# Performance work log

Measured on AMD Instinct MI355X. Metric: run time of the kernel, lower is better.

## Reference

```python
import jax, jax.numpy as jnp
import numpy as np

B, S, DIN = 1, 2048, 4096
H, KV, DH = 32, 8, 128          # num_heads, num_kv_groups, head_dim
G = H // KV                      # group_size


def setup_inputs() -> dict:
    key = jax.random.key(0)
    ks = jax.random.split(key, 6)
    input_tensor = jax.random.normal(ks[0], (B, S, DIN), jnp.float32)
    # boolean mask: True = masked out. Causal upper-triangular mask.
    attention_mask = jnp.triu(jnp.ones((S, S), bool), k=1)[None, None]
    # RoPE tables (context_len, head_dim), rotate-half layout
    inv_freq = 1.0 / (10000.0 ** (jnp.arange(0, DH, 2, dtype=jnp.float32) / DH))
    ang = jnp.arange(S, dtype=jnp.float32)[:, None] * inv_freq[None, :]  # (S, DH/2)
    ang = jnp.concatenate([ang, ang], axis=-1)                            # (S, DH)
    cos, sin = jnp.cos(ang), jnp.sin(ang)
    scale = 0.02
    Wq = jax.random.normal(ks[1], (DIN, H * DH), jnp.float32) * scale
    Wk = jax.random.normal(ks[2], (DIN, KV * DH), jnp.float32) * scale
    Wv = jax.random.normal(ks[3], (DIN, KV * DH), jnp.float32) * scale
    Wo = jax.random.normal(ks[4], (H * DH, DIN), jnp.float32) * scale
    return {"input_tensor": input_tensor, "attention_mask": attention_mask,
            "cos": cos, "sin": sin, "Wq": Wq, "Wk": Wk, "Wv": Wv, "Wo": Wo}


def _rope(t, cos, sin):
    # t: (B, heads, S, DH); cos/sin: (S, DH)
    t1, t2 = jnp.split(t, 2, axis=-1)
    rot = jnp.concatenate([-t2, t1], axis=-1)
    return t * cos[None, None] + rot * sin[None, None]


def reference(input_tensor, attention_mask, cos, sin, Wq, Wk, Wv, Wo):
    b, s, _ = input_tensor.shape
    q = (input_tensor @ Wq).reshape(b, s, H, DH).transpose(0, 2, 1, 3)   # (B,H,S,DH)
    k = (input_tensor @ Wk).reshape(b, s, KV, DH).transpose(0, 2, 1, 3)  # (B,KV,S,DH)
    v = (input_tensor @ Wv).reshape(b, s, KV, DH).transpose(0, 2, 1, 3)
    q = _rope(q, cos, sin)
    k = _rope(k, cos, sin)
    # GQA: duplicate each kv head across its group of query heads
    k = jnp.repeat(k, G, axis=1)  # (B,H,S,DH)
    v = jnp.repeat(v, G, axis=1)
    scores = jnp.einsum('bhqd,bhkd->bhqk', q, k)
    scores = jnp.where(attention_mask, -jnp.inf, scores)
    weights = jax.nn.softmax(scores / np.float32(np.sqrt(DH)), axis=-1)
    ctx = jnp.einsum('bhqk,bhkd->bhqd', weights, v)
    ctx = ctx.transpose(0, 2, 1, 3).reshape(b, s, H * DH)
    return ctx @ Wo
```

## Files before the change

### kernel.cpp

```cpp
#include <hip/hip_runtime.h>
#include <hip/hip_bf16.h>
#include <stdint.h>
#include <stddef.h>

typedef __attribute__((ext_vector_type(8))) short bf16x8;
typedef __attribute__((ext_vector_type(8))) unsigned short u16x8;
typedef __attribute__((ext_vector_type(4))) float f32x4;
typedef __attribute__((ext_vector_type(16))) float f32x16;

#define MFMA16(a, b, c) __builtin_amdgcn_mfma_f32_16x16x32_bf16((a), (b), (c), 0, 0, 0)
#define MFMA32(a, b, c) __builtin_amdgcn_mfma_f32_32x32x16_bf16((a), (b), (c), 0, 0, 0)

__device__ __forceinline__ unsigned short f2b(float f) {
  union { float f; unsigned u; } v; v.f = f;
  unsigned r = v.u + 0x7fffu + ((v.u >> 16) & 1u);
  return (unsigned short)(r >> 16);
}
__device__ __forceinline__ float b2f(unsigned short h) {
  union { unsigned u; float f; } v; v.u = ((unsigned)h) << 16;
  return v.f;
}

__device__ __forceinline__ void gload_lds16(const void* g, void* l) {
  __builtin_amdgcn_global_load_lds((const __attribute__((address_space(1))) void*)g,
                                   (__attribute__((address_space(3))) void*)l, 16, 0, 0);
}

__global__ void k_transpose_f32_bf16(const float* __restrict__ in,
                                     unsigned short* __restrict__ out,
                                     int K, int N) {
  __shared__ float tile[64][65];
  const int kb = blockIdx.x * 64;
  const int nb = blockIdx.y * 64;
  const int t = threadIdx.x;
  const int c4 = (t & 15) * 4;
  const int rr = t >> 4;
#pragma unroll
  for (int i = 0; i < 4; ++i) {
    int r = rr + i * 16;
    float4 v = *reinterpret_cast<const float4*>(in + (size_t)(kb + r) * N + nb + c4);
    tile[r][c4 + 0] = v.x; tile[r][c4 + 1] = v.y;
    tile[r][c4 + 2] = v.z; tile[r][c4 + 3] = v.w;
  }
  __syncthreads();
#pragma unroll
  for (int i = 0; i < 4; ++i) {
    int n = rr + i * 16;
    ushort4 w;
    w.x = f2b(tile[c4 + 0][n]); w.y = f2b(tile[c4 + 1][n]);
    w.z = f2b(tile[c4 + 2][n]); w.w = f2b(tile[c4 + 3][n]);
    *reinterpret_cast<ushort4*>(out + (size_t)(nb + n) * K + kb + c4) = w;
  }
}

__global__ void k_f32_to_bf16(const float* __restrict__ in, unsigned short* __restrict__ out) {
  size_t i = ((size_t)blockIdx.x * blockDim.x + threadIdx.x) * 4;
  float4 v = *reinterpret_cast<const float4*>(in + i);
  ushort4 w; w.x = f2b(v.x); w.y = f2b(v.y); w.z = f2b(v.z); w.w = f2b(v.w);
  *reinterpret_cast<ushort4*>(out + i) = w;
}

template <bool OUT_F32>
__global__ void __launch_bounds__(256, 2)
k_gemm(const unsigned short* __restrict__ A, const unsigned short* __restrict__ Bt,
       void* __restrict__ C, int M, int N, int K) {
  __shared__ unsigned short As[128 * 32];
  __shared__ unsigned short Bs[128 * 32];
  const int nbm = M >> 7;
  const int per = ((M >> 7) * (N >> 7)) >> 3;
  const int wg  = (blockIdx.x & 7) * per + (blockIdx.x >> 3);
  const int m0 = (wg % nbm) * 128;
  const int n0 = (wg / nbm) * 128;
  const int tid = threadIdx.x;
  const int lane = tid & 63;
  const int w = tid >> 6;
  const int wr = w >> 1, wc = w & 1;
  const int cl = lane & 15, rg = lane >> 4;
  const int ko = rg * 8;

  f32x4 acc[4][4] = {};

  for (int k0 = 0; k0 < K; k0 += 32) {
#pragma unroll
    for (int i = 0; i < 2; ++i) {
      int c = i * 256 + tid;
      gload_lds16(A + (size_t)(m0 + (c >> 2)) * K + k0 + (c & 3) * 8, As + c * 8);
    }
#pragma unroll
    for (int i = 0; i < 2; ++i) {
      int c = i * 256 + tid;
      gload_lds16(Bt + (size_t)(n0 + (c >> 2)) * K + k0 + (c & 3) * 8, Bs + c * 8);
    }
    __syncthreads();
    bf16x8 a[4], b[4];
#pragma unroll
    for (int mi = 0; mi < 4; ++mi)
      a[mi] = *reinterpret_cast<const bf16x8*>(As + (wr * 64 + mi * 16 + cl) * 32 + ko);
#pragma unroll
    for (int ni = 0; ni < 4; ++ni)
      b[ni] = *reinterpret_cast<const bf16x8*>(Bs + (wc * 64 + ni * 16 + cl) * 32 + ko);
#pragma unroll
    for (int mi = 0; mi < 4; ++mi)
#pragma unroll
      for (int ni = 0; ni < 4; ++ni)
        acc[mi][ni] = MFMA16(a[mi], b[ni], acc[mi][ni]);
    __syncthreads();
  }
#pragma unroll
  for (int mi = 0; mi < 4; ++mi)
#pragma unroll
    for (int ni = 0; ni < 4; ++ni) {
      int row = m0 + wr * 64 + mi * 16 + rg * 4;
      int col = n0 + wc * 64 + ni * 16 + cl;
#pragma unroll
      for (int r = 0; r < 4; ++r) {
        float v = acc[mi][ni][r];
        if (OUT_F32) ((float*)C)[(size_t)(row + r) * N + col] = v;
        else         ((unsigned short*)C)[(size_t)(row + r) * N + col] = f2b(v);
      }
    }
}

__global__ void k_rope(const unsigned short* __restrict__ Cpre,
                       const float* __restrict__ cosb, const float* __restrict__ sinb,
                       unsigned short* __restrict__ Qr, unsigned short* __restrict__ Kr) {
  const int s = blockIdx.x;
  const int hh = blockIdx.y * 2 + (threadIdx.x >> 7);
  const int d = threadIdx.x & 127;
  const int col = (hh < 32) ? hh * 128 + d : 4096 + (hh - 32) * 128 + d;
  float t = b2f(Cpre[(size_t)s * 6144 + col]);
  const int dp = (d < 64) ? d + 64 : d - 64;
  float tp = b2f(Cpre[(size_t)s * 6144 + (col - d + dp)]);
  float rot = (d < 64) ? -tp : tp;
  float o = t * cosb[s * 128 + d] + rot * sinb[s * 128 + d];
  if (hh < 32) {
    Qr[((size_t)hh * 2048 + s) * 128 + d] = f2b(o * 0.08838834764831845f);
  } else {
    Kr[((size_t)(hh - 32) * 2048 + s) * 128 + d] = f2b(o);
  }
}

__global__ void k_transpose_v(const unsigned short* __restrict__ Cpre,
                              unsigned short* __restrict__ Vt) {
  __shared__ unsigned short tile[64][72];
  const int sb = blockIdx.x * 64;
  const int db = blockIdx.y * 64;
  const int kv = blockIdx.z;
  const int t = threadIdx.x;
#pragma unroll
  for (int i = 0; i < 2; ++i) {
    int sl = i * 32 + (t >> 3);
    int d8 = (t & 7) * 8;
    const unsigned short* src = Cpre + (size_t)(sb + sl) * 6144 + 5120 + kv * 128 + db + d8;
    ushort4 v0 = *reinterpret_cast<const ushort4*>(src);
    ushort4 v1 = *reinterpret_cast<const ushort4*>(src + 4);
    *reinterpret_cast<ushort4*>(&tile[sl][d8]) = v0;
    *reinterpret_cast<ushort4*>(&tile[sl][d8 + 4]) = v1;
  }
  __syncthreads();
#pragma unroll
  for (int i = 0; i < 2; ++i) {
    int dl = i * 32 + (t >> 3);
    int s8 = (t & 7) * 8;
    ushort4 w0, w1;
    w0.x = tile[s8 + 0][dl]; w0.y = tile[s8 + 1][dl]; w0.z = tile[s8 + 2][dl]; w0.w = tile[s8 + 3][dl];
    w1.x = tile[s8 + 4][dl]; w1.y = tile[s8 + 5][dl]; w1.z = tile[s8 + 6][dl]; w1.w = tile[s8 + 7][dl];
    unsigned short* dst = Vt + ((size_t)kv * 128 + db + dl) * 2048 + sb + s8;
    *reinterpret_cast<ushort4*>(dst) = w0;
    *reinterpret_cast<ushort4*>(dst + 4) = w1;
  }
}

__global__ void __launch_bounds__(256, 2)
k_attn(const unsigned short* __restrict__ Qr, const unsigned short* __restrict__ Kr,
       const unsigned short* __restrict__ Vt, unsigned short* __restrict__ ctx) {
  __shared__ unsigned short Ks[64 * 128];
  __shared__ unsigned short Vs[128 * 64];
  const int bid = blockIdx.x;
  const int kv = bid & 7;
  const int hd = kv * 4 + ((bid >> 3) & 3);
  const int qb = 15 - (bid >> 5);
  const int q0 = qb * 128;
  const int tid = threadIdx.x;
  const int l = tid & 63;
  const int w = tid >> 6;
  const int i5 = l & 31;
  const int h  = l >> 5;
  const int qg = q0 + w * 16 + (i5 & 15) + (i5 >> 4) * 64;

  const unsigned short* Kbase = Kr + (size_t)kv * 2048 * 128;
  const unsigned short* Vbase = Vt + (size_t)kv * 128 * 2048;

  bf16x8 qf[8];
#pragma unroll
  for (int s = 0; s < 8; ++s)
    qf[s] = *reinterpret_cast<const bf16x8*>(
        Qr + ((size_t)hd * 2048 + qg) * 128 + s * 16 + h * 8);

  f32x16 po[4] = {};
  float mrow = -1e30f, lrow = 0.f;

  const int krr = tid >> 4, kcc = (tid & 15) * 8;
  const int vrr = tid >> 3, vcc = (tid & 7) * 8;

  u16x8 kst[4], vst[4];
#pragma unroll
  for (int ii = 0; ii < 4; ++ii)
    kst[ii] = *reinterpret_cast<const u16x8*>(Kbase + (size_t)(ii * 16 + krr) * 128 + kcc);
#pragma unroll
  for (int ii = 0; ii < 4; ++ii)
    vst[ii] = *reinterpret_cast<const u16x8*>(Vbase + (size_t)(ii * 32 + vrr) * 2048 + vcc);

  const int jmax = 2 * qb + 2;
  for (int j = 0; j < jmax; ++j) {
    asm volatile("" ::: "memory");
    __builtin_amdgcn_s_barrier();
    asm volatile("" ::: "memory");
#pragma unroll
    for (int ii = 0; ii < 4; ++ii) {
      int row = ii * 16 + krr;
      *reinterpret_cast<u16x8*>((char*)Ks + ((row * 256 + kcc * 2) ^ ((row & 7) << 4))) = kst[ii];
    }
#pragma unroll
    for (int ii = 0; ii < 4; ++ii) {
      int row = ii * 32 + vrr;
      *reinterpret_cast<u16x8*>((char*)Vs + ((row * 128 + vcc * 2) ^ ((row & 7) << 4))) = vst[ii];
    }
    const int jn = (j + 1 < jmax) ? j + 1 : j;
#pragma unroll
    for (int ii = 0; ii < 4; ++ii)
      kst[ii] = *reinterpret_cast<const u16x8*>(
          Kbase + (size_t)(jn * 64 + ii * 16 + krr) * 128 + kcc);
#pragma unroll
    for (int ii = 0; ii < 4; ++ii)
      vst[ii] = *reinterpret_cast<const u16x8*>(
          Vbase + (size_t)(ii * 32 + vrr) * 2048 + jn * 64 + vcc);
    asm volatile("s_waitcnt lgkmcnt(0)" ::: "memory");
    __builtin_amdgcn_s_barrier();
    asm volatile("" ::: "memory");

    f32x16 sa[2] = {};
    __builtin_amdgcn_s_setprio(1);
#pragma unroll
    for (int ni = 0; ni < 2; ++ni) {
      const int row = ni * 32 + i5;
      const int swz = (row & 7) << 4;
#pragma unroll
      for (int s = 0; s < 8; ++s) {
        bf16x8 kf = *reinterpret_cast<const bf16x8*>(
            (const char*)Ks + ((row * 256 + s * 32 + h * 16) ^ swz));
        sa[ni] = MFMA32(kf, qf[s], sa[ni]);
      }
    }
    __builtin_amdgcn_s_setprio(0);

    if (j >= 2 * qb) {
#pragma unroll
      for (int ni = 0; ni < 2; ++ni) {
        const int kvb = j * 64 + ni * 32 + 4 * h;
#pragma unroll
        for (int r = 0; r < 16; ++r) {
          int kvg = kvb + (r & 3) + 8 * (r >> 2);
          if (kvg > qg) sa[ni][r] = -__builtin_inff();
        }
      }
    }

    float pmax = sa[0][0];
#pragma unroll
    for (int r = 1; r < 16; ++r) pmax = fmaxf(pmax, sa[0][r]);
#pragma unroll
    for (int r = 0; r < 16; ++r) pmax = fmaxf(pmax, sa[1][r]);
    pmax = fmaxf(pmax, __shfl_xor(pmax, 32));

    if (!__all(pmax <= mrow + 8.0f)) {
      float mnew = fmaxf(mrow, pmax);
      float sf = __expf(mrow - mnew);
#pragma unroll
      for (int d = 0; d < 4; ++d)
#pragma unroll
        for (int r = 0; r < 16; ++r) po[d][r] *= sf;
      lrow *= sf;
      mrow = mnew;
    }

    float rs = 0.f;
#pragma unroll
    for (int ni = 0; ni < 2; ++ni)
#pragma unroll
      for (int r = 0; r < 16; ++r) {
        float p = __expf(sa[ni][r] - mrow);
        sa[ni][r] = p;
        rs += p;
      }
    rs += __shfl_xor(rs, 32);
    lrow += rs;

    bf16x8 pfrag[4];
#pragma unroll
    for (int ni = 0; ni < 2; ++ni) {
      unsigned wd[8];
#pragma unroll
      for (int c = 0; c < 4; ++c)
#pragma unroll
        for (int ii = 0; ii < 2; ++ii)
          wd[c * 2 + ii] = (unsigned)f2b(sa[ni][4 * c + 2 * ii]) |
                           ((unsigned)f2b(sa[ni][4 * c + 2 * ii + 1]) << 16);
#pragma unroll
      for (int k2 = 0; k2 < 2; ++k2) {
        unsigned e0 = wd[(2 * k2) * 2 + 0], e1 = wd[(2 * k2) * 2 + 1];
        unsigned o0 = wd[(2 * k2 + 1) * 2 + 0], o1 = wd[(2 * k2 + 1) * 2 + 1];
        unsigned pe0 = (unsigned)__shfl_xor((int)e0, 32);
        unsigned pe1 = (unsigned)__shfl_xor((int)e1, 32);
        unsigned po0 = (unsigned)__shfl_xor((int)o0, 32);
        unsigned po1 = (unsigned)__shfl_xor((int)o1, 32);
        union { unsigned u[4]; bf16x8 v; } uu;
        uu.u[0] = h ? po0 : e0;
        uu.u[1] = h ? po1 : e1;
        uu.u[2] = h ? o0 : pe0;
        uu.u[3] = h ? o1 : pe1;
        pfrag[ni * 2 + k2] = uu.v;
      }
    }

    __builtin_amdgcn_s_setprio(1);
#pragma unroll
    for (int d = 0; d < 4; ++d) {
      const int row0 = d * 32 + i5;
      const int swz = (row0 & 7) << 4;
#pragma unroll
      for (int ks = 0; ks < 4; ++ks) {
        bf16x8 vf = *reinterpret_cast<const bf16x8*>(
            (const char*)Vs + ((row0 * 128 + ks * 32 + h * 16) ^ swz));
        po[d] = MFMA32(vf, pfrag[ks], po[d]);
      }
    }
    __builtin_amdgcn_s_setprio(0);
  }

  const float inv = 1.0f / lrow;
#pragma unroll
  for (int d = 0; d < 4; ++d)
#pragma unroll
    for (int c = 0; c < 4; ++c) {
      ushort4 st;
      st.x = f2b(po[d][4 * c + 0] * inv);
      st.y = f2b(po[d][4 * c + 1] * inv);
      st.z = f2b(po[d][4 * c + 2] * inv);
      st.w = f2b(po[d][4 * c + 3] * inv);
      *reinterpret_cast<ushort4*>(
          ctx + (size_t)qg * 4096 + hd * 128 + d * 32 + 8 * c + 4 * h) = st;
    }
}

extern "C" void kernel_launch(void* const* d_in, const int* in_sizes, int n_in,
                              void* d_out, int out_size, void* d_ws, size_t ws_size,
                              hipStream_t stream) {
  const float* X    = (const float*)d_in[0];
  const float* cosb = (const float*)d_in[2];
  const float* sinb = (const float*)d_in[3];
  const float* Wq   = (const float*)d_in[4];
  const float* Wk   = (const float*)d_in[5];
  const float* Wv   = (const float*)d_in[6];
  const float* Wo   = (const float*)d_in[7];

  char* ws = (char*)d_ws;
  unsigned short* WT   = (unsigned short*)(ws + 0);
  unsigned short* Xb   = (unsigned short*)(ws + 50331648ull);
  unsigned short* Cpre = (unsigned short*)(ws + 67108864ull);
  unsigned short* Qr   = (unsigned short*)(ws + 92274688ull);
  unsigned short* Kr   = (unsigned short*)(ws + 109051904ull);
  unsigned short* Vt   = (unsigned short*)(ws + 113246208ull);
  unsigned short* ctx  = Cpre;

  k_transpose_f32_bf16<<<dim3(64, 64), 256, 0, stream>>>(Wq, WT, 4096, 4096);
  k_transpose_f32_bf16<<<dim3(64, 16), 256, 0, stream>>>(Wk, WT + (size_t)4096 * 4096, 4096, 1024);
  k_transpose_f32_bf16<<<dim3(64, 16), 256, 0, stream>>>(Wv, WT + (size_t)5120 * 4096, 4096, 1024);
  k_f32_to_bf16<<<8192, 256, 0, stream>>>(X, Xb);

  k_gemm<false><<<768, 256, 0, stream>>>(Xb, WT, Cpre, 2048, 6144, 4096);

  k_rope<<<dim3(2048, 20), 256, 0, stream>>>(Cpre, cosb, sinb, Qr, Kr);
  k_transpose_v<<<dim3(32, 2, 8), 256, 0, stream>>>(Cpre, Vt);

  k_transpose_f32_bf16<<<dim3(64, 64), 256, 0, stream>>>(Wo, WT, 4096, 4096);

  k_attn<<<512, 256, 0, stream>>>(Qr, Kr, Vt, ctx);

  k_gemm<true><<<512, 256, 0, stream>>>(ctx, WT, d_out, 2048, 4096, 4096);
}
```

Before: 357.3 us.

## Double-buffer attention K/V tiles via direct global-to-LDS loads; merge QKV transposes

The attention kernel now stages K/V tiles straight into double-buffered LDS with global_load_lds. The XOR swizzle moves to the global source address, and a partial vmcnt wait lets the next tile's load overlap the current tile's compute. This removes the register round-trip and the explicit LDS stores, at the cost of doubled LDS use (64KB per block), which may reduce occupancy. Separately, the three Wq/Wk/Wv transpose launches are merged into one kernel to cut launch overhead.

```diff
diff --git a/kernel.cpp b/kernel.cpp
--- a/kernel.cpp
+++ b/kernel.cpp
@@ -24,6 +24,36 @@
 __device__ __forceinline__ void gload_lds16(const void* g, void* l) {
   __builtin_amdgcn_global_load_lds((const __attribute__((address_space(1))) void*)g,
                                    (__attribute__((address_space(3))) void*)l, 16, 0, 0);
+}
+
+__global__ void k_transpose_qkv(const float* __restrict__ Wq, const float* __restrict__ Wk,
+                                const float* __restrict__ Wv, unsigned short* __restrict__ out) {
+  __shared__ float tile[64][65];
+  const int kb = blockIdx.x * 64;
+  const int nbg = blockIdx.y * 64;
+  const float* src; int srcN, nb;
+  if (nbg < 4096)      { src = Wq; srcN = 4096; nb = nbg; }
+  else if (nbg < 5120) { src = Wk; srcN = 1024; nb = nbg - 4096; }
+  else                 { src = Wv; srcN = 1024; nb = nbg - 5120; }
+  const int t = threadIdx.x;
+  const int c4 = (t & 15) * 4;
+  const int rr = t >> 4;
+#pragma unroll
+  for (int i = 0; i < 4; ++i) {
+    int r = rr + i * 16;
+    float4 v = *reinterpret_cast<const float4*>(src + (size_t)(kb + r) * srcN + nb + c4);
+    tile[r][c4 + 0] = v.x; tile[r][c4 + 1] = v.y;
+    tile[r][c4 + 2] = v.z; tile[r][c4 + 3] = v.w;
+  }
+  __syncthreads();
+#pragma unroll
+  for (int i = 0; i < 4; ++i) {
+    int n = rr + i * 16;
+    ushort4 w;
+    w.x = f2b(tile[c4 + 0][n]); w.y = f2b(tile[c4 + 1][n]);
+    w.z = f2b(tile[c4 + 2][n]); w.w = f2b(tile[c4 + 3][n]);
+    *reinterpret_cast<ushort4*>(out + (size_t)(nbg + n) * 4096 + kb + c4) = w;
+  }
 }
 
 __global__ void k_transpose_f32_bf16(const float* __restrict__ in,
@@ -174,8 +204,8 @@
 __global__ void __launch_bounds__(256, 2)
 k_attn(const unsigned short* __restrict__ Qr, const unsigned short* __restrict__ Kr,
        const unsigned short* __restrict__ Vt, unsigned short* __restrict__ ctx) {
-  __shared__ unsigned short Ks[64 * 128];
-  __shared__ unsigned short Vs[128 * 64];
+  __shared__ unsigned short Ks[2][64 * 128];
+  __shared__ unsigned short Vs[2][128 * 64];
   const int bid = blockIdx.x;
   const int kv = bid & 7;
   const int hd = kv * 4 + ((bid >> 3) & 3);
@@ -188,8 +218,8 @@
   const int h  = l >> 5;
   const int qg = q0 + w * 16 + (i5 & 15) + (i5 >> 4) * 64;
 
-  const unsigned short* Kbase = Kr + (size_t)kv * 2048 * 128;
-  const unsigned short* Vbase = Vt + (size_t)kv * 128 * 2048;
+  const char* Kbase = (const char*)(Kr + (size_t)kv * 2048 * 128);
+  const char* Vbase = (const char*)(Vt + (size_t)kv * 128 * 2048);
 
   bf16x8 qf[8];
 #pragma unroll
@@ -200,44 +230,43 @@
   f32x16 po[4] = {};
   float mrow = -1e30f, lrow = 0.f;
 
-  const int krr = tid >> 4, kcc = (tid & 15) * 8;
-  const int vrr = tid >> 3, vcc = (tid & 7) * 8;
-
-  u16x8 kst[4], vst[4];
-#pragma unroll
-  for (int ii = 0; ii < 4; ++ii)
-    kst[ii] = *reinterpret_cast<const u16x8*>(Kbase + (size_t)(ii * 16 + krr) * 128 + kcc);
-#pragma unroll
-  for (int ii = 0; ii < 4; ++ii)
-    vst[ii] = *reinterpret_cast<const u16x8*>(Vbase + (size_t)(ii * 32 + vrr) * 2048 + vcc);
+  const int krow = tid >> 4;
+  const int kcol = (tid & 15) * 16;
+  const int vrow = tid >> 3;
+  const int vcol = (tid & 7) * 16;
+
+#define STAGE_KV(JT, BUF)                                                      \
+  {                                                                            \
+    _Pragma("unroll")                                                          \
+    for (int ii = 0; ii < 4; ++ii) {                                           \
+      int row = ii * 16 + krow;                                                \
+      gload_lds16(Kbase + (size_t)((JT) * 64 + row) * 256 +                    \
+                      (kcol ^ ((row & 7) << 4)),                               \
+                  (char*)Ks[BUF] + row * 256 + kcol);                          \
+    }                                                                          \
+    _Pragma("unroll")                                                          \
+    for (int ii = 0; ii < 4; ++ii) {                                           \
+      int row = ii * 32 + vrow;                                                \
+      gload_lds16(Vbase + (size_t)row * 4096 + (JT) * 128 +                    \
+                      (vcol ^ ((row & 7) << 4)),                               \
+                  (char*)Vs[BUF] + row * 128 + vcol);                          \
+    }                                                                          \
+  }
+
+  STAGE_KV(0, 0)
 
   const int jmax = 2 * qb + 2;
   for (int j = 0; j < jmax; ++j) {
-    asm volatile("" ::: "memory");
+    const int cur = j & 1;
+    const int jn = (j + 1 < jmax) ? j + 1 : j;
+    STAGE_KV(jn, cur ^ 1)
+    asm volatile("s_waitcnt vmcnt(8)" ::: "memory");
+    __builtin_amdgcn_sched_barrier(0);
     __builtin_amdgcn_s_barrier();
-    asm volatile("" ::: "memory");
-#pragma unroll
-    for (int ii = 0; ii < 4; ++ii) {
-      int row = ii * 16 + krr;
-      *reinterpret_cast<u16x8*>((char*)Ks + ((row * 256 + kcc * 2) ^ ((row & 7) << 4))) = kst[ii];
-    }
-#pragma unroll
-    for (int ii = 0; ii < 4; ++ii) {
-      int row = ii * 32 + vrr;
-      *reinterpret_cast<u16x8*>((char*)Vs + ((row * 128 + vcc * 2) ^ ((row & 7) << 4))) = vst[ii];
-    }
-    const int jn = (j + 1 < jmax) ? j + 1 : j;
-#pragma unroll
-    for (int ii = 0; ii < 4; ++ii)
-      kst[ii] = *reinterpret_cast<const u16x8*>(
-          Kbase + (size_t)(jn * 64 + ii * 16 + krr) * 128 + kcc);
-#pragma unroll
-    for (int ii = 0; ii < 4; ++ii)
-      vst[ii] = *reinterpret_cast<const u16x8*>(
-          Vbase + (size_t)(ii * 32 + vrr) * 2048 + jn * 64 + vcc);
-    asm volatile("s_waitcnt lgkmcnt(0)" ::: "memory");
-    __builtin_amdgcn_s_barrier();
-    asm volatile("" ::: "memory");
+    __builtin_amdgcn_sched_barrier(0);
+
+    const unsigned short* Kc = Ks[cur];
+    const unsigned short* Vc = Vs[cur];
 
     f32x16 sa[2] = {};
     __builtin_amdgcn_s_setprio(1);
@@ -248,7 +277,7 @@
 #pragma unroll
       for (int s = 0; s < 8; ++s) {
         bf16x8 kf = *reinterpret_cast<const bf16x8*>(
-            (const char*)Ks + ((row * 256 + s * 32 + h * 16) ^ swz));
+            (const char*)Kc + ((row * 256 + s * 32 + h * 16) ^ swz));
         sa[ni] = MFMA32(kf, qf[s], sa[ni]);
       }
     }
@@ -331,12 +360,17 @@
 #pragma unroll
       for (int ks = 0; ks < 4; ++ks) {
         bf16x8 vf = *reinterpret_cast<const bf16x8*>(
-            (const char*)Vs + ((row0 * 128 + ks * 32 + h * 16) ^ swz));
+            (const char*)Vc + ((row0 * 128 + ks * 32 + h * 16) ^ swz));
         po[d] = MFMA32(vf, pfrag[ks], po[d]);
       }
     }
     __builtin_amdgcn_s_setprio(0);
-  }
+
+    __builtin_amdgcn_sched_barrier(0);
+    __builtin_amdgcn_s_barrier();
+    __builtin_amdgcn_sched_barrier(0);
+  }
+#undef STAGE_KV
 
   const float inv = 1.0f / lrow;
 #pragma unroll
@@ -373,9 +407,7 @@
   unsigned short* Vt   = (unsigned short*)(ws + 113246208ull);
   unsigned short* ctx  = Cpre;
 
-  k_transpose_f32_bf16<<<dim3(64, 64), 256, 0, stream>>>(Wq, WT, 4096, 4096);
-  k_transpose_f32_bf16<<<dim3(64, 16), 256, 0, stream>>>(Wk, WT + (size_t)4096 * 4096, 4096, 1024);
-  k_transpose_f32_bf16<<<dim3(64, 16), 256, 0, stream>>>(Wv, WT + (size_t)5120 * 4096, 4096, 1024);
+  k_transpose_qkv<<<dim3(64, 96), 256, 0, stream>>>(Wq, Wk, Wv, WT);
   k_f32_to_bf16<<<8192, 256, 0, stream>>>(X, Xb);
 
   k_gemm<false><<<768, 256, 0, stream>>>(Xb, WT, Cpre, 2048, 6144, 4096);
```

Measured after the change: 349.0 us. 2.3% less time.
